# Kernel tuning notes

Measured on AMD Instinct MI355X. Metric: run time of the kernel, lower is better.

The kernel has to match this reference:

```python
import jax, jax.numpy as jnp
import numpy as np

B, S, D, H, DK, FF = 2, 2048, 1024, 16, 64, 4096
EPS = 1e-6


def _layernorm(x, g, b):
    m = jnp.mean(x, axis=-1, keepdims=True)
    v = jnp.mean((x - m) ** 2, axis=-1, keepdims=True)
    return (x - m) * jax.lax.rsqrt(v + EPS) * g + b


def setup_inputs() -> dict:
    key = jax.random.key(0)
    ks = jax.random.split(key, 20)
    sc = 0.02
    rn = lambda k, sh: (jax.random.normal(k, sh, jnp.float32) * sc)
    return {
        "inputs": jax.random.normal(ks[0], (B, S, D), jnp.float32),
        "wq": rn(ks[1], (D, H * DK)), "bq": jnp.zeros((H * DK,), jnp.float32),
        "wk": rn(ks[2], (D, H * DK)), "bk": jnp.zeros((H * DK,), jnp.float32),
        "wv": rn(ks[3], (D, H * DK)), "bv": jnp.zeros((H * DK,), jnp.float32),
        "wo": rn(ks[4], (H * DK, D)), "bo": jnp.zeros((D,), jnp.float32),
        "ln1_g": jnp.ones((D,), jnp.float32), "ln1_b": jnp.zeros((D,), jnp.float32),
        "wi0": rn(ks[5], (D, FF)), "bi0": jnp.zeros((FF,), jnp.float32),
        "wi1": rn(ks[6], (D, FF)), "bi1": jnp.zeros((FF,), jnp.float32),
        "wff": rn(ks[7], (FF, D)), "bff": jnp.zeros((D,), jnp.float32),
        "ln2_g": jnp.ones((D,), jnp.float32), "ln2_b": jnp.zeros((D,), jnp.float32),
    }


def reference(inputs, wq, bq, wk, bk, wv, bv, wo, bo, ln1_g, ln1_b,
              wi0, bi0, wi1, bi1, wff, bff, ln2_g, ln2_b):
    # --- pre-norm MHA block ---
    h = _layernorm(inputs, ln1_g, ln1_b)
    q = (h @ wq + bq).reshape(B, S, H, DK)
    k = (h @ wk + bk).reshape(B, S, H, DK)
    v = (h @ wv + bv).reshape(B, S, H, DK)
    scores = jnp.einsum('bqhd,bkhd->bhqk', q, k) / jnp.sqrt(jnp.float32(DK))
    attn = jax.nn.softmax(scores, axis=-1)                 # [B,H,S,S]
    ctx = jnp.einsum('bhqk,bkhd->bqhd', attn, v).reshape(B, S, H * DK)
    h1 = inputs + (ctx @ wo + bo)
    # --- pre-norm GeGLU FFN block ---
    h2 = _layernorm(h1, ln2_g, ln2_b)
    hg = jax.nn.gelu(h2 @ wi0 + bi0, approximate=False)
    hl = h2 @ wi1 + bi1
    out = h1 + ((hg * hl) @ wff + bff)
    return out, attn
```

## Files before the change

### kernel.cpp

```cpp
#include <hip/hip_runtime.h>
#include <hip/hip_bf16.h>
#include <cstdint>

#define DEV __device__ __forceinline__

typedef __bf16 bf16_t;
typedef __bf16 bf16x8 __attribute__((ext_vector_type(8)));
typedef __bf16 bf16x4 __attribute__((ext_vector_type(4)));
typedef float  f32x4  __attribute__((ext_vector_type(4)));

constexpr int Bb = 2, Ss = 2048, Dd = 1024, Hh = 16, DKk = 64, FFf = 4096;
constexpr int TOK = Bb * Ss;
constexpr float LN_EPS = 1e-6f;

DEV void g2l16(const void* g, void* l) {
    __builtin_amdgcn_global_load_lds(
        (const __attribute__((address_space(1))) unsigned int*)g,
        (__attribute__((address_space(3))) unsigned int*)l, 16, 0, 0);
}

#define WAITCNT(N) asm volatile("s_waitcnt vmcnt(" #N ")" ::: "memory")
#define SCHEDB() __builtin_amdgcn_sched_barrier(0)

__global__ __launch_bounds__(256)
void transpose_all(const float* __restrict__ wq, const float* __restrict__ wk,
                   const float* __restrict__ wv, const float* __restrict__ wo,
                   const float* __restrict__ wi0, const float* __restrict__ wi1,
                   const float* __restrict__ wff,
                   bf16_t* wqT, bf16_t* wkT, bf16_t* wvT, bf16_t* woT,
                   bf16_t* wi0T, bf16_t* wi1T, bf16_t* wffT) {
    __shared__ float t[32][33];
    const int id = blockIdx.x;
    const float* src; bf16_t* dst; int K, N, tt;
    if (id < 4096) {
        const int w = id >> 10; tt = id & 1023; K = 1024; N = 1024;
        src = w == 0 ? wq : w == 1 ? wk : w == 2 ? wv : wo;
        dst = w == 0 ? wqT : w == 1 ? wkT : w == 2 ? wvT : woT;
    } else if (id < 12288) {
        const int w = (id - 4096) >> 12; tt = (id - 4096) & 4095; K = 1024; N = 4096;
        src = w ? wi1 : wi0; dst = w ? wi1T : wi0T;
    } else {
        tt = id - 12288; K = 4096; N = 1024;
        src = wff; dst = wffT;
    }
    const int ntn = N >> 5;
    const int n0 = (tt % ntn) * 32, k0 = (tt / ntn) * 32;
    const int tx = threadIdx.x & 31, ty = threadIdx.x >> 5;
#pragma unroll
    for (int i = 0; i < 4; ++i)
        t[ty + 8 * i][tx] = src[(size_t)(k0 + ty + 8 * i) * N + n0 + tx];
    __syncthreads();
#pragma unroll
    for (int i = 0; i < 4; ++i)
        dst[(size_t)(n0 + ty + 8 * i) * K + k0 + tx] = (bf16_t)t[tx][ty + 8 * i];
}

__global__ __launch_bounds__(256)
void concat3(const float* __restrict__ a, const float* __restrict__ b,
             const float* __restrict__ c, float* __restrict__ o) {
    const int i = blockIdx.x * 256 + threadIdx.x;
    o[i] = a[i]; o[1024 + i] = b[i]; o[2048 + i] = c[i];
}

__global__ __launch_bounds__(256)
void ln_fwd(const float* __restrict__ x, const float* __restrict__ g,
            const float* __restrict__ b, bf16_t* __restrict__ out) {
    __shared__ float red[8];
    const int row = blockIdx.x, tid = threadIdx.x;
    const float4 v = ((const float4*)(x + (size_t)row * Dd))[tid];
    float s  = v.x + v.y + v.z + v.w;
    float sq = v.x * v.x + v.y * v.y + v.z * v.z + v.w * v.w;
#pragma unroll
    for (int o = 32; o; o >>= 1) { s += __shfl_xor(s, o); sq += __shfl_xor(sq, o); }
    if ((tid & 63) == 0) { red[tid >> 6] = s; red[4 + (tid >> 6)] = sq; }
    __syncthreads();
    s  = red[0] + red[1] + red[2] + red[3];
    sq = red[4] + red[5] + red[6] + red[7];
    const float mean = s * (1.f / Dd);
    const float var  = sq * (1.f / Dd) - mean * mean;
    const float rs   = rsqrtf(var + LN_EPS);
    const float4 gv = ((const float4*)g)[tid];
    const float4 bv = ((const float4*)b)[tid];
    bf16x4 o4;
    o4[0] = (bf16_t)((v.x - mean) * rs * gv.x + bv.x);
    o4[1] = (bf16_t)((v.y - mean) * rs * gv.y + bv.y);
    o4[2] = (bf16_t)((v.z - mean) * rs * gv.z + bv.z);
    o4[3] = (bf16_t)((v.w - mean) * rs * gv.w + bv.w);
    ((bf16x4*)(out + (size_t)row * Dd))[tid] = o4;
}

template <int EPI>
DEV void gemm_epi(float val, int gr, int gc, int N, size_t zofs,
                  void* outp, void* out2, void* out3, const float* resid) {
    if constexpr (EPI == 0) {
        ((bf16_t*)outp)[(size_t)gr * N + gc] = (bf16_t)val;
    } else if constexpr (EPI == 1) {
        const size_t idx = (size_t)gr * N + gc;
        ((float*)outp)[idx] = val + resid[idx];
    } else if constexpr (EPI == 4) {
        ((float*)outp)[zofs + (size_t)gr * N + gc] = val;
    } else {
        const int sel = gc >> 10, col = gc & 1023;
        if (sel == 0) {
            ((bf16_t*)outp)[(size_t)gr * 1024 + col] = (bf16_t)val;
        } else if (sel == 1) {
            ((bf16_t*)out2)[(size_t)gr * 1024 + col] = (bf16_t)val;
        } else {
            const int bb = gr >> 11, sS = gr & 2047;
            ((bf16_t*)out3)[((size_t)bb << 21) + ((size_t)col << 11) + sS] = (bf16_t)val;
        }
    }
}

template <int BM, int BN, int EPI>
__global__ __launch_bounds__(256)
void gemm_t(const bf16_t* __restrict__ A, const bf16_t* __restrict__ Bt,
            const float* __restrict__ bias, const float* __restrict__ resid,
            void* __restrict__ outp, void* __restrict__ out2,
            void* __restrict__ out3, int M, int N, int K, int ld) {
    constexpr int WM = BM / 2, WN = BN / 2;
    constexpr int MI = WM / 16, NI = WN / 16;
    constexpr int CA = BM / 32, CB = BN / 32;
    __shared__ bf16_t As[BM * 64];
    __shared__ bf16_t Bs[BN * 64];
    const int tid = threadIdx.x;
    const int lane = tid & 63;
    const int wave = tid >> 6;
    const int wr = wave >> 1, wc = wave & 1;
    const int m0 = blockIdx.y * BM, n0 = blockIdx.x * BN;
    const int koff = blockIdx.z * K;
    const size_t zofs = (size_t)blockIdx.z * M * N;
    const int lr = lane & 15, lg = lane >> 4;

    const f32x4 z0 = {0.f, 0.f, 0.f, 0.f};
    f32x4 acc[MI][NI];
#pragma unroll
    for (int i = 0; i < MI; ++i)
#pragma unroll
        for (int j = 0; j < NI; ++j) acc[i][j] = z0;

    for (int k0 = 0; k0 < K; k0 += 64) {
#pragma unroll
        for (int c = 0; c < CA; ++c) {
            const int lin = c * 256 + tid;
            const int row = lin >> 3, col = (lin & 7) * 8;
            g2l16(A + (size_t)(m0 + row) * ld + koff + k0 + col, (char*)As + lin * 16);
        }
#pragma unroll
        for (int c = 0; c < CB; ++c) {
            const int lin = c * 256 + tid;
            const int row = lin >> 3, col = (lin & 7) * 8;
            g2l16(Bt + (size_t)(n0 + row) * ld + koff + k0 + col, (char*)Bs + lin * 16);
        }
        __syncthreads();

        bf16x8 af[2][MI], bw[2][NI];
#pragma unroll
        for (int kk = 0; kk < 2; ++kk)
#pragma unroll
            for (int mi = 0; mi < MI; ++mi)
                af[kk][mi] = *(const bf16x8*)(As + (wr * WM + mi * 16 + lr) * 64 +
                                              kk * 32 + lg * 8);
#pragma unroll
        for (int kk = 0; kk < 2; ++kk)
#pragma unroll
            for (int ni = 0; ni < NI; ++ni)
                bw[kk][ni] = *(const bf16x8*)(Bs + (wc * WN + ni * 16 + lr) * 64 +
                                              kk * 32 + lg * 8);
#pragma unroll
        for (int mi = 0; mi < MI; ++mi)
#pragma unroll
            for (int ni = 0; ni < NI; ++ni) {
                acc[mi][ni] = __builtin_amdgcn_mfma_f32_16x16x32_bf16(
                    af[0][mi], bw[0][ni], acc[mi][ni], 0, 0, 0);
                acc[mi][ni] = __builtin_amdgcn_mfma_f32_16x16x32_bf16(
                    af[1][mi], bw[1][ni], acc[mi][ni], 0, 0, 0);
            }
        __syncthreads();
    }

#pragma unroll
    for (int mi = 0; mi < MI; ++mi)
#pragma unroll
        for (int ni = 0; ni < NI; ++ni) {
            const int gc = n0 + wc * WN + ni * 16 + lr;
            const int gr0 = m0 + wr * WM + mi * 16 + lg * 4;
            const float bvl = (EPI == 4) ? 0.f : bias[gc];
#pragma unroll
            for (int r = 0; r < 4; ++r)
                gemm_epi<EPI>(acc[mi][ni][r] + bvl, gr0 + r, gc, N, zofs,
                              outp, out2, out3, resid);
        }
}

__global__ __launch_bounds__(256)
void reduce2(const float* __restrict__ part, const float* __restrict__ h1,
             const float* __restrict__ bff, float* __restrict__ out) {
    const int row = blockIdx.x, tid = threadIdx.x;
    const size_t idx = (size_t)row * 1024 + tid * 4;
    const float4 a = *(const float4*)(part + idx);
    const float4 b = *(const float4*)(part + (size_t)4096 * 1024 + idx);
    const float4 r = *(const float4*)(h1 + idx);
    const float4 bv = *(const float4*)(bff + tid * 4);
    float4 o;
    o.x = a.x + b.x + r.x + bv.x;
    o.y = a.y + b.y + r.y + bv.y;
    o.z = a.z + b.z + r.z + bv.z;
    o.w = a.w + b.w + r.w + bv.w;
    *(float4*)(out + idx) = o;
}

__global__ __launch_bounds__(256)
void gemm_geglu(const bf16_t* __restrict__ A, const bf16_t* __restrict__ Bg,
                const bf16_t* __restrict__ Bl, const float* __restrict__ bi0,
                const float* __restrict__ bi1, bf16_t* __restrict__ gout) {
    __shared__ bf16_t As[128 * 64];
    __shared__ bf16_t Bgs[64 * 64];
    __shared__ bf16_t Bls[64 * 64];
    const int tid = threadIdx.x;
    const int lane = tid & 63;
    const int wave = tid >> 6;
    const int wr = wave >> 1, wc = wave & 1;
    const int m0 = blockIdx.y * 128, n0 = blockIdx.x * 64;
    const int lr = lane & 15, lg = lane >> 4;

    const f32x4 z0 = {0.f, 0.f, 0.f, 0.f};
    f32x4 ag[4][2], al[4][2];
#pragma unroll
    for (int i = 0; i < 4; ++i)
#pragma unroll
        for (int j = 0; j < 2; ++j) { ag[i][j] = z0; al[i][j] = z0; }

    for (int k0 = 0; k0 < 1024; k0 += 64) {
#pragma unroll
        for (int c = 0; c < 4; ++c) {
            const int lin = c * 256 + tid;
            const int row = lin >> 3, col = (lin & 7) * 8;
            g2l16(A + (size_t)(m0 + row) * 1024 + k0 + col, (char*)As + lin * 16);
        }
#pragma unroll
        for (int c = 0; c < 2; ++c) {
            const int lin = c * 256 + tid;
            const int row = lin >> 3, col = (lin & 7) * 8;
            g2l16(Bg + (size_t)(n0 + row) * 1024 + k0 + col, (char*)Bgs + lin * 16);
        }
#pragma unroll
        for (int c = 0; c < 2; ++c) {
            const int lin = c * 256 + tid;
            const int row = lin >> 3, col = (lin & 7) * 8;
            g2l16(Bl + (size_t)(n0 + row) * 1024 + k0 + col, (char*)Bls + lin * 16);
        }
        __syncthreads();

        bf16x8 af[2][4], bg[2][2], bl[2][2];
#pragma unroll
        for (int kk = 0; kk < 2; ++kk) {
#pragma unroll
            for (int mi = 0; mi < 4; ++mi)
                af[kk][mi] = *(const bf16x8*)(As + (wr * 64 + mi * 16 + lr) * 64 +
                                              kk * 32 + lg * 8);
#pragma unroll
            for (int ni = 0; ni < 2; ++ni) {
                bg[kk][ni] = *(const bf16x8*)(Bgs + (wc * 32 + ni * 16 + lr) * 64 +
                                              kk * 32 + lg * 8);
                bl[kk][ni] = *(const bf16x8*)(Bls + (wc * 32 + ni * 16 + lr) * 64 +
                                              kk * 32 + lg * 8);
            }
        }
#pragma unroll
        for (int mi = 0; mi < 4; ++mi)
#pragma unroll
            for (int ni = 0; ni < 2; ++ni) {
#pragma unroll
                for (int kk = 0; kk < 2; ++kk) {
                    ag[mi][ni] = __builtin_amdgcn_mfma_f32_16x16x32_bf16(
                        af[kk][mi], bg[kk][ni], ag[mi][ni], 0, 0, 0);
                    al[mi][ni] = __builtin_amdgcn_mfma_f32_16x16x32_bf16(
                        af[kk][mi], bl[kk][ni], al[mi][ni], 0, 0, 0);
                }
            }
        __syncthreads();
    }

#pragma unroll
    for (int mi = 0; mi < 4; ++mi)
#pragma unroll
        for (int ni = 0; ni < 2; ++ni) {
            const int gc = n0 + wc * 32 + ni * 16 + lr;
            const int gr0 = m0 + wr * 64 + mi * 16 + lg * 4;
            const float b0 = bi0[gc], b1 = bi1[gc];
#pragma unroll
            for (int r = 0; r < 4; ++r) {
                const float x = ag[mi][ni][r] + b0;
                const float y = al[mi][ni][r] + b1;
                const float ge = 0.5f * x * (1.f + erff(x * 0.70710678118654752f));
                gout[(size_t)(gr0 + r) * 4096 + gc] = (bf16_t)(ge * y);
            }
        }
}

__global__ __launch_bounds__(512)
void attn_fused(const bf16_t* __restrict__ q, const bf16_t* __restrict__ k,
                const bf16_t* __restrict__ vT, float* __restrict__ attn,
                bf16_t* __restrict__ ctx) {
    __shared__ bf16_t Ks[3][64 * 64];
    __shared__ bf16_t Vs[3][64 * 64];
    const int tid = threadIdx.x, lane = tid & 63, wave = tid >> 6;
    const int lr = lane & 15, lg = lane >> 4;
    int blk = blockIdx.x;
    blk = (blk & 7) * 64 + (blk >> 3);
    const int qc = blk & 15, bh = blk >> 4;
    const int b = bh >> 4, h = bh & 15;
    const int q0 = qc * 128 + wave * 16;
    const size_t base = (size_t)b * (Ss * 1024) + h * 64;
    constexpr float SCL = 0.125f * 1.4426950408889634f;
    const f32x4 z0 = {0.f, 0.f, 0.f, 0.f};

    const int st_r8 = lane >> 3;
    const int st_row = wave * 8 + st_r8;
    const int st_c0 = (lane & 7) ^ (st_r8 & 3) ^ ((wave & 1) << 2);

    const bf16x8 aq0 = *(const bf16x8*)(q + base + (size_t)(q0 + lr) * 1024 + lg * 8);
    const bf16x8 aq1 = *(const bf16x8*)(q + base + (size_t)(q0 + lr) * 1024 + 32 + lg * 8);
    const bf16_t* kb = k + base;
    const bf16_t* vb_base = vT + ((size_t)bh * 64) * Ss;

#define STAGE_K(kt_, buf_)                                                       \
    g2l16(kb + (size_t)((kt_) * 64 + st_row) * 1024 + st_c0 * 8,                 \
          &Ks[buf_][wave * 512]);
#define STAGE_V(kt_, buf_)                                                       \
    g2l16(vb_base + (size_t)st_row * Ss + (kt_) * 64 + st_c0 * 8,                \
          &Vs[buf_][wave * 512]);

    f32x4 ea = z0, eb = z0;
    STAGE_K(0, 0);
    STAGE_K(1, 1);
    for (int kt = 0; kt < 32; ++kt) {
        const int buf = kt % 3;
        if (kt == 31) { WAITCNT(0); } else { WAITCNT(1); }
        SCHEDB();
        __builtin_amdgcn_s_barrier();
        SCHEDB();
        f32x4 sa[4];
        __builtin_amdgcn_s_setprio(1);
#pragma unroll
        for (int ct = 0; ct < 4; ++ct) {
            const int ar = ct * 16 + lr;
            const int hz = (ar & 3) | (((ar >> 3) & 1) << 2);
            bf16x8 k0 = *(const bf16x8*)&Ks[buf][ar * 64 + (lg ^ hz) * 8];
            bf16x8 k1 = *(const bf16x8*)&Ks[buf][ar * 64 + (((4 + lg) ^ hz)) * 8];
            sa[ct] = __builtin_amdgcn_mfma_f32_16x16x32_bf16(k0, aq0, z0, 0, 0, 0);
            sa[ct] = __builtin_amdgcn_mfma_f32_16x16x32_bf16(k1, aq1, sa[ct], 0, 0, 0);
        }
        __builtin_amdgcn_s_setprio(0);
#pragma unroll
        for (int r = 0; r < 4; ++r) {
            ea[r] += exp2f(sa[0][r] * SCL) + exp2f(sa[1][r] * SCL);
            eb[r] += exp2f(sa[2][r] * SCL) + exp2f(sa[3][r] * SCL);
        }
        if (kt + 2 < 32) STAGE_K(kt + 2, (kt + 2) % 3);
    }
    float e = ((ea[0] + ea[1]) + (ea[2] + ea[3])) + ((eb[0] + eb[1]) + (eb[2] + eb[3]));
    e += __shfl_xor(e, 16);
    e += __shfl_xor(e, 32);
    const float invl = 1.f / e;

    f32x4 cacc[4];
#pragma unroll
    for (int nd = 0; nd < 4; ++nd) cacc[nd] = z0;

    float* attn_base = attn + ((size_t)bh * Ss + q0 + lr) * Ss;

    __builtin_amdgcn_s_barrier();
    SCHEDB();

    STAGE_K(0, 0); STAGE_V(0, 0);
    STAGE_K(1, 1); STAGE_V(1, 1);
    for (int kt = 0; kt < 32; ++kt) {
        const int buf = kt % 3;
        if (kt == 0) { WAITCNT(2); }
        else if (kt == 31) { WAITCNT(4); }
        else { WAITCNT(6); }
        SCHEDB();
        __builtin_amdgcn_s_barrier();
        SCHEDB();
#pragma unroll
        for (int kp = 0; kp < 2; ++kp) {
            bf16x8 pa;
            __builtin_amdgcn_s_setprio(1);
#pragma unroll
            for (int ch = 0; ch < 2; ++ch) {
                const int pr = kp * 32 + (lr >> 2) * 8 + ch * 4 + (lr & 3);
                const int hz = (pr & 3) | (((pr >> 3) & 1) << 2);
                bf16x8 k0 = *(const bf16x8*)&Ks[buf][pr * 64 + (lg ^ hz) * 8];
                bf16x8 k1 = *(const bf16x8*)&Ks[buf][pr * 64 + (((4 + lg) ^ hz)) * 8];
                f32x4 sb = __builtin_amdgcn_mfma_f32_16x16x32_bf16(k0, aq0, z0, 0, 0, 0);
                sb = __builtin_amdgcn_mfma_f32_16x16x32_bf16(k1, aq1, sb, 0, 0, 0);
                float4 p;
                p.x = exp2f(sb[0] * SCL) * invl;
                p.y = exp2f(sb[1] * SCL) * invl;
                p.z = exp2f(sb[2] * SCL) * invl;
                p.w = exp2f(sb[3] * SCL) * invl;
                *(float4*)(attn_base + kt * 64 + kp * 32 + lg * 8 + ch * 4) = p;
                pa[ch * 4 + 0] = (bf16_t)p.x;
                pa[ch * 4 + 1] = (bf16_t)p.y;
                pa[ch * 4 + 2] = (bf16_t)p.z;
                pa[ch * 4 + 3] = (bf16_t)p.w;
            }
#pragma unroll
            for (int nd = 0; nd < 4; ++nd) {
                const int vr = nd * 16 + lr;
                const int hv = (vr & 3) | (((vr >> 3) & 1) << 2);
                bf16x8 vb = *(const bf16x8*)&Vs[buf][vr * 64 + (((kp * 4 + lg) ^ hv)) * 8];
                cacc[nd] = __builtin_amdgcn_mfma_f32_16x16x32_bf16(pa, vb, cacc[nd], 0, 0, 0);
            }
            __builtin_amdgcn_s_setprio(0);
        }
        if (kt + 2 < 32) {
            const int nb = (kt + 2) % 3;
            STAGE_K(kt + 2, nb);
            STAGE_V(kt + 2, nb);
        }
    }
#pragma unroll
    for (int nd = 0; nd < 4; ++nd)
#pragma unroll
        for (int r = 0; r < 4; ++r)
            ctx[((size_t)b * Ss + q0 + lg * 4 + r) * 1024 + h * 64 + nd * 16 + lr] =
                (bf16_t)cacc[nd][r];
#undef STAGE_K
#undef STAGE_V
}

extern "C" void kernel_launch(void* const* d_in, const int* in_sizes, int n_in,
                              void* d_out, int out_size, void* d_ws, size_t ws_size,
                              hipStream_t stream) {
    const float* inp  = (const float*)d_in[0];
    const float* wq   = (const float*)d_in[1];
    const float* bq   = (const float*)d_in[2];
    const float* wk   = (const float*)d_in[3];
    const float* bk   = (const float*)d_in[4];
    const float* wv   = (const float*)d_in[5];
    const float* bv   = (const float*)d_in[6];
    const float* wo   = (const float*)d_in[7];
    const float* bo   = (const float*)d_in[8];
    const float* ln1g = (const float*)d_in[9];
    const float* ln1b = (const float*)d_in[10];
    const float* wi0  = (const float*)d_in[11];
    const float* bi0  = (const float*)d_in[12];
    const float* wi1  = (const float*)d_in[13];
    const float* bi1  = (const float*)d_in[14];
    const float* wff  = (const float*)d_in[15];
    const float* bff  = (const float*)d_in[16];
    const float* ln2g = (const float*)d_in[17];
    const float* ln2b = (const float*)d_in[18];

    const size_t M1 = 1u << 20;
    bf16_t* wsb  = (bf16_t*)d_ws;
    bf16_t* wqT  = wsb + 0 * M1;
    bf16_t* wkT  = wsb + 1 * M1;
    bf16_t* wvT  = wsb + 2 * M1;
    bf16_t* woT  = wsb + 3 * M1;
    bf16_t* wi0T = wsb + 4 * M1;
    bf16_t* wi1T = wsb + 8 * M1;
    bf16_t* wffT = wsb + 12 * M1;
    bf16_t* hbuf = wsb + 16 * M1;
    bf16_t* qbuf = wsb + 20 * M1;
    bf16_t* kbuf = wsb + 24 * M1;
    bf16_t* vTb  = wsb + 28 * M1;
    bf16_t* ctxb = wsb + 32 * M1;
    float*  h1   = (float*)(wsb + 36 * M1);
    bf16_t* gbuf = wsb + 44 * M1;
    float*  part = (float*)(wsb + 20 * M1);
    float*  cb   = (float*)(wsb + 60 * M1);

    float* out  = (float*)d_out;
    float* attn = out + (size_t)TOK * Dd;

    transpose_all<<<16384, 256, 0, stream>>>(wq, wk, wv, wo, wi0, wi1, wff,
                                             wqT, wkT, wvT, woT, wi0T, wi1T, wffT);

    concat3<<<4, 256, 0, stream>>>(bq, bk, bv, cb);

    ln_fwd<<<TOK, 256, 0, stream>>>(inp, ln1g, ln1b, hbuf);

    gemm_t<128, 128, 3><<<dim3(24, 32), 256, 0, stream>>>(
        hbuf, wqT, cb, nullptr, qbuf, kbuf, vTb, TOK, 3072, 1024, 1024);

    attn_fused<<<Bb * Hh * (Ss / 128), 512, 0, stream>>>(qbuf, kbuf, vTb, attn, ctxb);

    gemm_t<64, 64, 1><<<dim3(16, 64), 256, 0, stream>>>(
        ctxb, woT, bo, inp, h1, nullptr, nullptr, TOK, 1024, 1024, 1024);

    ln_fwd<<<TOK, 256, 0, stream>>>(h1, ln2g, ln2b, hbuf);

    gemm_geglu<<<dim3(64, 32), 256, 0, stream>>>(hbuf, wi0T, wi1T, bi0, bi1, gbuf);

    gemm_t<128, 64, 4><<<dim3(16, 32, 2), 256, 0, stream>>>(
        gbuf, wffT, bff, nullptr, part, nullptr, nullptr, TOK, 1024, 2048, 4096);

    reduce2<<<4096, 256, 0, stream>>>(part, h1, bff, out);
}
```

Baseline: 478.0 us.

## Fold bias concat into transpose, split FFN-down GEMM 4-way, defer attn stores

The bias concatenation moves into an extra block of the weight-transpose kernel, which removes one launch. The FFN down-projection GEMM now uses 128x128 tiles with a 4-way split-K instead of 64-column tiles with a 2-way split. Partials go to two buffers and are summed by a 4-input reduce kernel, so the larger tiles keep a similar grid size at the cost of more partial-sum traffic. In the attention kernel, the fp32 probability stores are moved after the PV MFMAs so the write latency overlaps compute. p23 aliases cb, but cb is consumed before the GEMM runs.

```diff
diff --git a/kernel.cpp b/kernel.cpp
--- a/kernel.cpp
+++ b/kernel.cpp
@@ -28,9 +28,20 @@
                    const float* __restrict__ wi0, const float* __restrict__ wi1,
                    const float* __restrict__ wff,
                    bf16_t* wqT, bf16_t* wkT, bf16_t* wvT, bf16_t* woT,
-                   bf16_t* wi0T, bf16_t* wi1T, bf16_t* wffT) {
+                   bf16_t* wi0T, bf16_t* wi1T, bf16_t* wffT,
+                   const float* __restrict__ bq, const float* __restrict__ bk,
+                   const float* __restrict__ bv, float* __restrict__ cb) {
     __shared__ float t[32][33];
     const int id = blockIdx.x;
+    if (id == 16384) {
+        const int tid = threadIdx.x;
+#pragma unroll
+        for (int i = 0; i < 4; ++i) {
+            const int j = i * 256 + tid;
+            cb[j] = bq[j]; cb[1024 + j] = bk[j]; cb[2048 + j] = bv[j];
+        }
+        return;
+    }
     const float* src; bf16_t* dst; int K, N, tt;
     if (id < 4096) {
         const int w = id >> 10; tt = id & 1023; K = 1024; N = 1024;
@@ -53,13 +64,6 @@
 #pragma unroll
     for (int i = 0; i < 4; ++i)
         dst[(size_t)(n0 + ty + 8 * i) * K + k0 + tx] = (bf16_t)t[tx][ty + 8 * i];
-}
-
-__global__ __launch_bounds__(256)
-void concat3(const float* __restrict__ a, const float* __restrict__ b,
-             const float* __restrict__ c, float* __restrict__ o) {
-    const int i = blockIdx.x * 256 + threadIdx.x;
-    o[i] = a[i]; o[1024 + i] = b[i]; o[2048 + i] = c[i];
 }
 
 __global__ __launch_bounds__(256)
@@ -129,7 +133,8 @@
     const int wr = wave >> 1, wc = wave & 1;
     const int m0 = blockIdx.y * BM, n0 = blockIdx.x * BN;
     const int koff = blockIdx.z * K;
-    const size_t zofs = (size_t)blockIdx.z * M * N;
+    const size_t zofs = (size_t)(blockIdx.z & 1) * M * N;
+    void* outsel = (EPI == 4 && blockIdx.z >= 2) ? out2 : outp;
     const int lr = lane & 15, lg = lane >> 4;
 
     const f32x4 z0 = {0.f, 0.f, 0.f, 0.f};
@@ -189,24 +194,28 @@
 #pragma unroll
             for (int r = 0; r < 4; ++r)
                 gemm_epi<EPI>(acc[mi][ni][r] + bvl, gr0 + r, gc, N, zofs,
-                              outp, out2, out3, resid);
+                              outsel, out2, out3, resid);
         }
 }
 
 __global__ __launch_bounds__(256)
-void reduce2(const float* __restrict__ part, const float* __restrict__ h1,
-             const float* __restrict__ bff, float* __restrict__ out) {
+void reduce4(const float* __restrict__ p01, const float* __restrict__ p23,
+             const float* __restrict__ h1, const float* __restrict__ bff,
+             float* __restrict__ out) {
+    constexpr size_t MN = (size_t)4096 * 1024;
     const int row = blockIdx.x, tid = threadIdx.x;
     const size_t idx = (size_t)row * 1024 + tid * 4;
-    const float4 a = *(const float4*)(part + idx);
-    const float4 b = *(const float4*)(part + (size_t)4096 * 1024 + idx);
+    const float4 a = *(const float4*)(p01 + idx);
+    const float4 b = *(const float4*)(p01 + MN + idx);
+    const float4 c = *(const float4*)(p23 + idx);
+    const float4 d = *(const float4*)(p23 + MN + idx);
     const float4 r = *(const float4*)(h1 + idx);
     const float4 bv = *(const float4*)(bff + tid * 4);
     float4 o;
-    o.x = a.x + b.x + r.x + bv.x;
-    o.y = a.y + b.y + r.y + bv.y;
-    o.z = a.z + b.z + r.z + bv.z;
-    o.w = a.w + b.w + r.w + bv.w;
+    o.x = a.x + b.x + c.x + d.x + r.x + bv.x;
+    o.y = a.y + b.y + c.y + d.y + r.y + bv.y;
+    o.z = a.z + b.z + c.z + d.z + r.z + bv.z;
+    o.w = a.w + b.w + c.w + d.w + r.w + bv.w;
     *(float4*)(out + idx) = o;
 }
 
@@ -387,6 +396,7 @@
 #pragma unroll
         for (int kp = 0; kp < 2; ++kp) {
             bf16x8 pa;
+            float4 pst[2];
             __builtin_amdgcn_s_setprio(1);
 #pragma unroll
             for (int ch = 0; ch < 2; ++ch) {
@@ -401,7 +411,7 @@
                 p.y = exp2f(sb[1] * SCL) * invl;
                 p.z = exp2f(sb[2] * SCL) * invl;
                 p.w = exp2f(sb[3] * SCL) * invl;
-                *(float4*)(attn_base + kt * 64 + kp * 32 + lg * 8 + ch * 4) = p;
+                pst[ch] = p;
                 pa[ch * 4 + 0] = (bf16_t)p.x;
                 pa[ch * 4 + 1] = (bf16_t)p.y;
                 pa[ch * 4 + 2] = (bf16_t)p.z;
@@ -415,6 +425,9 @@
                 cacc[nd] = __builtin_amdgcn_mfma_f32_16x16x32_bf16(pa, vb, cacc[nd], 0, 0, 0);
             }
             __builtin_amdgcn_s_setprio(0);
+#pragma unroll
+            for (int ch = 0; ch < 2; ++ch)
+                *(float4*)(attn_base + kt * 64 + kp * 32 + lg * 8 + ch * 4) = pst[ch];
         }
         if (kt + 2 < 32) {
             const int nb = (kt + 2) % 3;
@@ -471,16 +484,16 @@
     bf16_t* ctxb = wsb + 32 * M1;
     float*  h1   = (float*)(wsb + 36 * M1);
     bf16_t* gbuf = wsb + 44 * M1;
-    float*  part = (float*)(wsb + 20 * M1);
+    float*  p01  = (float*)(wsb + 16 * M1);
+    float*  p23  = (float*)(wsb + 60 * M1);
     float*  cb   = (float*)(wsb + 60 * M1);
 
     float* out  = (float*)d_out;
     float* attn = out + (size_t)TOK * Dd;
 
-    transpose_all<<<16384, 256, 0, stream>>>(wq, wk, wv, wo, wi0, wi1, wff,
-                                             wqT, wkT, wvT, woT, wi0T, wi1T, wffT);
-
-    concat3<<<4, 256, 0, stream>>>(bq, bk, bv, cb);
+    transpose_all<<<16385, 256, 0, stream>>>(wq, wk, wv, wo, wi0, wi1, wff,
+                                             wqT, wkT, wvT, woT, wi0T, wi1T, wffT,
+                                             bq, bk, bv, cb);
 
     ln_fwd<<<TOK, 256, 0, stream>>>(inp, ln1g, ln1b, hbuf);
 
@@ -496,8 +509,8 @@
 
     gemm_geglu<<<dim3(64, 32), 256, 0, stream>>>(hbuf, wi0T, wi1T, bi0, bi1, gbuf);
 
-    gemm_t<128, 64, 4><<<dim3(16, 32, 2), 256, 0, stream>>>(
-        gbuf, wffT, bff, nullptr, part, nullptr, nullptr, TOK, 1024, 2048, 4096);
-
-    reduce2<<<4096, 256, 0, stream>>>(part, h1, bff, out);
-}
+    gemm_t<128, 128, 4><<<dim3(8, 32, 4), 256, 0, stream>>>(
+        gbuf, wffT, bff, nullptr, p01, p23, nullptr, TOK, 1024, 1024, 4096);
+
+    reduce4<<<4096, 256, 0, stream>>>(p01, p23, h1, bff, out);
+}
```

Result: slower. 500.9 us (+4.8%).
